# Kernel optimization log

Hardware: AMD Instinct MI355X
Metric: run time of the kernel (lower is better)

The kernel has to match this reference:

```python
import jax, jax.numpy as jnp
import numpy as np

DIM = 768


def setup_inputs() -> dict:
    key = jax.random.key(0)
    k1, k2, k3, k4, k5 = jax.random.split(key, 5)
    lines = jax.random.normal(k1, (32, 512, DIM), dtype=jnp.float32)
    videos = jax.random.normal(k2, (32, 128, DIM), dtype=jnp.float32)
    video_mask = jax.random.randint(k3, (32, 128), 0, 2, dtype=jnp.int32)
    # nn.Linear(dim, dim, bias=False) weights, applied as x @ W.T
    w_q = jax.random.normal(k4, (DIM, DIM), dtype=jnp.float32) * (DIM ** -0.5)
    w_k = jax.random.normal(k5, (DIM, DIM), dtype=jnp.float32) * (DIM ** -0.5)
    return {"lines": lines, "videos": videos, "video_mask": video_mask, "w_q": w_q, "w_k": w_k}


def reference(lines, videos, video_mask, w_q, w_k):
    scale = DIM ** -0.5
    q = jnp.einsum('bld,ed->ble', lines, w_q)   # (B, L, D)
    k = jnp.einsum('bvd,ed->bve', videos, w_k)  # (B, V, D)
    scores = jnp.einsum('bld,bvd->blv', q, k) * scale
    pad = (video_mask == 0)[:, None, :]          # (B, 1, V)
    scores = jnp.where(pad, jnp.float32(-1e9), scores)
    weights = jax.nn.softmax(scores, axis=-1)    # (B, L, V)
    return jnp.einsum('blv,bvd->bld', weights, videos)
```

## Files before the change

### kernel.cpp

```cpp
#include <hip/hip_runtime.h>

#define DIM 768
#define NB  32
#define LQ  512
#define NV  128

typedef unsigned short u16;
typedef unsigned int   u32;
typedef __bf16 bf16x8 __attribute__((ext_vector_type(8)));
typedef float  f32x4  __attribute__((ext_vector_type(4)));
typedef u16    u16x8  __attribute__((ext_vector_type(8)));
typedef u16    u16x4  __attribute__((ext_vector_type(4)));

typedef __attribute__((address_space(1))) const void gvoid;
typedef __attribute__((address_space(3))) void       svoid;

__device__ __forceinline__ u16 f2bf(float f) {
    u32 u = __float_as_uint(f);
    return (u16)((u + 0x7FFFu + ((u >> 16) & 1u)) >> 16);
}

__device__ __forceinline__ bf16x8 ld_frag(const u16* p) {
    return __builtin_bit_cast(bf16x8, *(const u16x8*)p);
}

__device__ __forceinline__ void gld16(const void* g, void* l) {
    __builtin_amdgcn_global_load_lds((gvoid*)g, (svoid*)l, 16, 0, 0);
}

#define NL_BLK 6144
#define NW_BLK 288

__device__ __forceinline__ void cvt_body(const float* __restrict__ src,
                                         u16* __restrict__ dst, int blk) {
    size_t i = (size_t)blk * 256 + threadIdx.x;
    float4 a = ((const float4*)src)[i * 2];
    float4 b = ((const float4*)src)[i * 2 + 1];
    u16x8 o = { f2bf(a.x), f2bf(a.y), f2bf(a.z), f2bf(a.w),
                f2bf(b.x), f2bf(b.y), f2bf(b.z), f2bf(b.w) };
    ((u16x8*)dst)[i] = o;
}

__global__ __launch_bounds__(256) void prep_kernel(const float* __restrict__ lines,
                                                   const float* __restrict__ w_q,
                                                   const float* __restrict__ w_k,
                                                   const float* __restrict__ videos,
                                                   u16* __restrict__ lbf,
                                                   u16* __restrict__ wqb,
                                                   u16* __restrict__ wkb,
                                                   u16* __restrict__ vt2,
                                                   u16* __restrict__ vbf) {
    __shared__ u16 T[64][136];
    const int bx = blockIdx.x;
    if (bx < NL_BLK)                 { cvt_body(lines, lbf, bx); return; }
    if (bx < NL_BLK + NW_BLK)        { cvt_body(w_q,   wqb, bx - NL_BLK); return; }
    if (bx < NL_BLK + 2 * NW_BLK)    { cvt_body(w_k,   wkb, bx - NL_BLK - NW_BLK); return; }

    const int v  = bx - (NL_BLK + 2 * NW_BLK);
    const int b  = v / 12;
    const int d0 = (v % 12) * 64;
    const int t  = threadIdx.x;
    const float* src = videos + (size_t)b * NV * DIM;
#pragma unroll
    for (int p = 0; p < 8; ++p) {
        int f  = t + p * 256;
        int vv = f >> 4;
        int c4 = f & 15;
        float4 x = *(const float4*)(src + (size_t)vv * DIM + d0 + c4 * 4);
        u16x4 o = { f2bf(x.x), f2bf(x.y), f2bf(x.z), f2bf(x.w) };
        T[c4 * 4 + 0][vv] = o[0];
        T[c4 * 4 + 1][vv] = o[1];
        T[c4 * 4 + 2][vv] = o[2];
        T[c4 * 4 + 3][vv] = o[3];
        *(u16x4*)(vbf + ((size_t)b * NV + vv) * DIM + d0 + c4 * 4) = o;
    }
    __syncthreads();
#pragma unroll
    for (int p = 0; p < 4; ++p) {
        int f  = t + p * 256;
        int dl = f >> 4;
        int v8 = f & 15;
        int d  = d0 + dl;
        int it = d >> 7, wv = (d >> 4) & 7, lnn = d & 15;
        int ks = v8 >> 2, qd = v8 & 3;
        int lane = qd * 16 + lnn;
        size_t off = ((((size_t)b * 6 + it) * 8 + wv) * 4 + ks) * 512 + lane * 8;
        *(u16x8*)(vt2 + off) = *(const u16x8*)&T[dl][v8 * 8];
    }
}

__global__ __launch_bounds__(512) void proj_kernel(const u16* __restrict__ A0,
                                                   const u16* __restrict__ W0,
                                                   u16* __restrict__ C0,
                                                   const u16* __restrict__ A1,
                                                   const u16* __restrict__ W1,
                                                   u16* __restrict__ C1) {
    __shared__ u16 sA[128][64];
    __shared__ u16 sB[128][64];
    const int t    = threadIdx.x;
    const int w    = t >> 6;
    const int lane = t & 63;
    const int quad = lane >> 4;
    const int ln   = lane & 15;

    const u16 *A, *W; u16 *C; int m0, n0;
    {
        int i = blockIdx.x;
        if (i < 768) { A = A0; W = W0; C = C0; }
        else         { A = A1; W = W1; C = C1; i -= 768; }
        int xcd = i & 7, s = i >> 3;
        m0 = ((s / 6) * 8 + xcd) * 128;
        n0 = (s % 6) * 128;
    }

    const int wr = (w >> 2) * 64;
    const int wc = (w & 3) * 32;
    const int srow   = lane >> 3;
    const int schunk = (lane & 7) ^ srow;

    f32x4 acc[4][2] = {};
#pragma unroll
    for (int ks = 0; ks < 12; ++ks) {
        __syncthreads();
#pragma unroll
        for (int p = 0; p < 2; ++p) {
            int rb = w * 16 + p * 8;
            gld16(A + (size_t)(m0 + rb + srow) * DIM + ks * 64 + schunk * 8, &sA[rb][0]);
            gld16(W + (size_t)(n0 + rb + srow) * DIM + ks * 64 + schunk * 8, &sB[rb][0]);
        }
        __syncthreads();
#pragma unroll
        for (int kk = 0; kk < 2; ++kk) {
            bf16x8 af[4], bfr[2];
#pragma unroll
            for (int i = 0; i < 4; ++i)
                af[i]  = ld_frag(&sA[wr + i * 16 + ln][((kk * 4 + quad) ^ (ln & 7)) * 8]);
#pragma unroll
            for (int j = 0; j < 2; ++j)
                bfr[j] = ld_frag(&sB[wc + j * 16 + ln][((kk * 4 + quad) ^ (ln & 7)) * 8]);
#pragma unroll
            for (int i = 0; i < 4; ++i)
#pragma unroll
                for (int j = 0; j < 2; ++j)
                    acc[i][j] = __builtin_amdgcn_mfma_f32_16x16x32_bf16(af[i], bfr[j], acc[i][j], 0, 0, 0);
        }
    }
#pragma unroll
    for (int i = 0; i < 4; ++i)
#pragma unroll
        for (int j = 0; j < 2; ++j)
#pragma unroll
            for (int r = 0; r < 4; ++r)
                C[(size_t)(m0 + wr + i * 16 + quad * 4 + r) * DIM + n0 + wc + j * 16 + ln] =
                    f2bf(acc[i][j][r]);
}

__global__ __launch_bounds__(512) void attn_kernel(const u16* __restrict__ Q,
                                                   const u16* __restrict__ K,
                                                   const u16* __restrict__ Vt2,
                                                   const int* __restrict__ mask,
                                                   float* __restrict__ out) {
    int b, l0;
    {
        int i = blockIdx.x;
        int xcd = i & 7, s = i >> 3;
        b  = (s >> 3) * 8 + xcd;
        l0 = (s & 7) * 64;
    }
    const int t    = threadIdx.x;
    const int w    = t >> 6;
    const int lane = t & 63;
    const int quad = lane >> 4;
    const int ln   = lane & 15;

    __shared__ union {
        struct { u16 q[64][64]; u16 k[128][64]; } st;
        float s[64][132];
    } uA;
    __shared__ union {
        struct { u16 q[64][64]; u16 k[128][64]; } st;
        u16 p[64][136];
    } uB;
    __shared__ float sBias[128];

    const u16* Qb = Q + ((size_t)b * LQ + l0) * DIM;
    const u16* Kb = K + (size_t)b * NV * DIM;
    if (t < NV) sBias[t] = mask[b * NV + t] ? 0.0f : -1e9f;

    const int srow   = lane >> 3;
    const int schunk = (lane & 7) ^ srow;

    auto stage = [&](int ks, int sel) {
        u16 (*q)[64] = sel ? uB.st.q : uA.st.q;
        u16 (*k)[64] = sel ? uB.st.k : uA.st.k;
        gld16(Qb + (size_t)(w * 8 + srow) * DIM + ks * 64 + schunk * 8, &q[w * 8][0]);
        gld16(Kb + (size_t)(w * 16 + srow) * DIM + ks * 64 + schunk * 8, &k[w * 16][0]);
        gld16(Kb + (size_t)(w * 16 + 8 + srow) * DIM + ks * 64 + schunk * 8, &k[w * 16 + 8][0]);
    };

    f32x4 accS[4] = {};
    stage(0, 0);
#pragma unroll
    for (int ks = 0; ks < 12; ++ks) {
        __syncthreads();
        if (ks < 11) stage(ks + 1, (ks + 1) & 1);
        u16 (*q)[64] = (ks & 1) ? uB.st.q : uA.st.q;
        u16 (*k)[64] = (ks & 1) ? uB.st.k : uA.st.k;
#pragma unroll
        for (int kk = 0; kk < 2; ++kk) {
            bf16x8 bfr = ld_frag(&k[w * 16 + ln][((kk * 4 + quad) ^ (ln & 7)) * 8]);
#pragma unroll
            for (int i = 0; i < 4; ++i) {
                bf16x8 af = ld_frag(&q[i * 16 + ln][((kk * 4 + quad) ^ (ln & 7)) * 8]);
                accS[i] = __builtin_amdgcn_mfma_f32_16x16x32_bf16(af, bfr, accS[i], 0, 0, 0);
            }
        }
    }
    __syncthreads();
    const float scale = 0.03608439182435161f;
#pragma unroll
    for (int i = 0; i < 4; ++i)
#pragma unroll
        for (int r = 0; r < 4; ++r)
            uA.s[i * 16 + quad * 4 + r][w * 16 + ln] = accS[i][r] * scale;
    __syncthreads();

    {
        const int row = t >> 3, seg = t & 7;
        float vals[16];
        float mx = -3.0e38f;
#pragma unroll
        for (int c = 0; c < 4; ++c) {
            float4 x  = *(const float4*)&uA.s[row][seg * 16 + c * 4];
            float4 bz = *(const float4*)&sBias[seg * 16 + c * 4];
            float a0 = x.x + bz.x, a1 = x.y + bz.y, a2 = x.z + bz.z, a3 = x.w + bz.w;
            vals[c * 4 + 0] = a0; vals[c * 4 + 1] = a1;
            vals[c * 4 + 2] = a2; vals[c * 4 + 3] = a3;
            mx = fmaxf(mx, fmaxf(fmaxf(a0, a1), fmaxf(a2, a3)));
        }
        mx = fmaxf(mx, __shfl_xor(mx, 1));
        mx = fmaxf(mx, __shfl_xor(mx, 2));
        mx = fmaxf(mx, __shfl_xor(mx, 4));
        float sum = 0.0f;
#pragma unroll
        for (int c = 0; c < 16; ++c) { float e = __expf(vals[c] - mx); vals[c] = e; sum += e; }
        sum += __shfl_xor(sum, 1);
        sum += __shfl_xor(sum, 2);
        sum += __shfl_xor(sum, 4);
        const float inv = 1.0f / sum;
        __syncthreads();
#pragma unroll
        for (int h = 0; h < 2; ++h) {
            u16x8 pk;
#pragma unroll
            for (int e = 0; e < 8; ++e) pk[e] = f2bf(vals[h * 8 + e] * inv);
            *(u16x8*)&uB.p[row][seg * 16 + h * 8] = pk;
        }
    }
    __syncthreads();

    bf16x8 paf[4][4];
#pragma unroll
    for (int i = 0; i < 4; ++i)
#pragma unroll
        for (int ks = 0; ks < 4; ++ks)
            paf[i][ks] = ld_frag(&uB.p[i * 16 + ln][ks * 32 + quad * 8]);

    const u16* V2 = Vt2 + (size_t)b * 6 * 8 * 4 * 512;
    float*     Ob = out + ((size_t)b * LQ + l0) * DIM;
    for (int it = 0; it < 6; ++it) {
        f32x4 accO[4] = {};
#pragma unroll
        for (int ks = 0; ks < 4; ++ks) {
            bf16x8 bv = ld_frag(V2 + (((size_t)(it * 8 + w)) * 4 + ks) * 512 + lane * 8);
#pragma unroll
            for (int i = 0; i < 4; ++i)
                accO[i] = __builtin_amdgcn_mfma_f32_16x16x32_bf16(paf[i][ks], bv, accO[i], 0, 0, 0);
        }
#pragma unroll
        for (int i = 0; i < 4; ++i)
#pragma unroll
            for (int r = 0; r < 4; ++r)
                Ob[(size_t)(i * 16 + quad * 4 + r) * DIM + it * 128 + w * 16 + ln] = accO[i][r];
    }
}

extern "C" void kernel_launch(void* const* d_in, const int* in_sizes, int n_in,
                              void* d_out, int out_size, void* d_ws, size_t ws_size,
                              hipStream_t stream) {
    const float* lines  = (const float*)d_in[0];
    const float* videos = (const float*)d_in[1];
    const int*   mask   = (const int*)d_in[2];
    const float* w_q    = (const float*)d_in[3];
    const float* w_k    = (const float*)d_in[4];
    float*       out    = (float*)d_out;

    u16* qw  = (u16*)d_ws;
    u16* kw  = qw  + (size_t)NB * LQ * DIM;
    u16* vt2 = kw  + (size_t)NB * NV * DIM;
    u16* lbf = vt2 + (size_t)NB * DIM * NV;
    u16* vbf = lbf + (size_t)NB * LQ * DIM;
    u16* wqb = vbf + (size_t)NB * NV * DIM;
    u16* wkb = wqb + (size_t)DIM * DIM;

    prep_kernel<<<NL_BLK + 2 * NW_BLK + 384, 256, 0, stream>>>(
        lines, w_q, w_k, videos, lbf, wqb, wkb, vt2, vbf);
    proj_kernel<<<960, 512, 0, stream>>>(lbf, wqb, qw, vbf, wkb, kw);
    attn_kernel<<<256, 512, 0, stream>>>(qw, kw, vt2, mask, out);
}
```

Before: 168.5 us.

## Fold Wq^T Wk into one matrix and project only videos

Scores are reassociated as lines · (Wq^T Wk · videos^T). A 768x768 combined weight is computed in the prep kernel from transposed fp32 tiles, then a smaller GEMM projects only the videos (B*128 rows) with that weight, and attention uses the raw bf16 lines as queries. This removes the large lines projection GEMM (B*512 rows). In exchange, the weight product is rounded to bf16, which adds a second rounding step that changes precision, and the few blocks computing the weight product may become a long tail in prep.

```diff
diff --git a/kernel.cpp b/kernel.cpp
--- a/kernel.cpp
+++ b/kernel.cpp
@@ -28,38 +28,92 @@
     __builtin_amdgcn_global_load_lds((gvoid*)g, (svoid*)l, 16, 0, 0);
 }
 
+#define W2_BLK 36
 #define NL_BLK 6144
-#define NW_BLK 288
-
-__device__ __forceinline__ void cvt_body(const float* __restrict__ src,
-                                         u16* __restrict__ dst, int blk) {
-    size_t i = (size_t)blk * 256 + threadIdx.x;
-    float4 a = ((const float4*)src)[i * 2];
-    float4 b = ((const float4*)src)[i * 2 + 1];
-    u16x8 o = { f2bf(a.x), f2bf(a.y), f2bf(a.z), f2bf(a.w),
-                f2bf(b.x), f2bf(b.y), f2bf(b.z), f2bf(b.w) };
-    ((u16x8*)dst)[i] = o;
-}
 
 __global__ __launch_bounds__(256) void prep_kernel(const float* __restrict__ lines,
                                                    const float* __restrict__ w_q,
                                                    const float* __restrict__ w_k,
                                                    const float* __restrict__ videos,
                                                    u16* __restrict__ lbf,
-                                                   u16* __restrict__ wqb,
-                                                   u16* __restrict__ wkb,
+                                                   u16* __restrict__ w2b,
                                                    u16* __restrict__ vt2,
                                                    u16* __restrict__ vbf) {
-    __shared__ u16 T[64][136];
+    __shared__ union {
+        u16 T[64][136];
+        struct { u16 q[128][72]; u16 k[128][72]; } w2s;
+    } uL;
     const int bx = blockIdx.x;
-    if (bx < NL_BLK)                 { cvt_body(lines, lbf, bx); return; }
-    if (bx < NL_BLK + NW_BLK)        { cvt_body(w_q,   wqb, bx - NL_BLK); return; }
-    if (bx < NL_BLK + 2 * NW_BLK)    { cvt_body(w_k,   wkb, bx - NL_BLK - NW_BLK); return; }
-
-    const int v  = bx - (NL_BLK + 2 * NW_BLK);
+    const int t  = threadIdx.x;
+
+    if (bx < W2_BLK) {
+        const int m0 = (bx / 6) * 128;
+        const int n0 = (bx % 6) * 128;
+        const int w    = t >> 6;
+        const int lane = t & 63;
+        const int quad = lane >> 4;
+        const int ln   = lane & 15;
+        const int wr   = (w >> 1) * 64;
+        const int wc   = (w & 1) * 64;
+        f32x4 acc[4][4] = {};
+        for (int ks = 0; ks < 12; ++ks) {
+            __syncthreads();
+            const int e0 = ks * 64;
+#pragma unroll
+            for (int p = 0; p < 8; ++p) {
+                int f  = t + p * 256;
+                int r  = f >> 5;
+                int c4 = f & 31;
+                float4 xq = *(const float4*)(w_q + (size_t)(e0 + r) * DIM + m0 + c4 * 4);
+                float4 xk = *(const float4*)(w_k + (size_t)(e0 + r) * DIM + n0 + c4 * 4);
+                uL.w2s.q[c4 * 4 + 0][r] = f2bf(xq.x);
+                uL.w2s.q[c4 * 4 + 1][r] = f2bf(xq.y);
+                uL.w2s.q[c4 * 4 + 2][r] = f2bf(xq.z);
+                uL.w2s.q[c4 * 4 + 3][r] = f2bf(xq.w);
+                uL.w2s.k[c4 * 4 + 0][r] = f2bf(xk.x);
+                uL.w2s.k[c4 * 4 + 1][r] = f2bf(xk.y);
+                uL.w2s.k[c4 * 4 + 2][r] = f2bf(xk.z);
+                uL.w2s.k[c4 * 4 + 3][r] = f2bf(xk.w);
+            }
+            __syncthreads();
+#pragma unroll
+            for (int kk = 0; kk < 2; ++kk) {
+                bf16x8 af[4], bfr[4];
+#pragma unroll
+                for (int i = 0; i < 4; ++i) af[i]  = ld_frag(&uL.w2s.q[wr + i * 16 + ln][kk * 32 + quad * 8]);
+#pragma unroll
+                for (int j = 0; j < 4; ++j) bfr[j] = ld_frag(&uL.w2s.k[wc + j * 16 + ln][kk * 32 + quad * 8]);
+#pragma unroll
+                for (int i = 0; i < 4; ++i)
+#pragma unroll
+                    for (int j = 0; j < 4; ++j)
+                        acc[i][j] = __builtin_amdgcn_mfma_f32_16x16x32_bf16(af[i], bfr[j], acc[i][j], 0, 0, 0);
+            }
+        }
+#pragma unroll
+        for (int i = 0; i < 4; ++i)
+#pragma unroll
+            for (int j = 0; j < 4; ++j)
+#pragma unroll
+                for (int r = 0; r < 4; ++r)
+                    w2b[(size_t)(m0 + wr + i * 16 + quad * 4 + r) * DIM + n0 + wc + j * 16 + ln] =
+                        f2bf(acc[i][j][r]);
+        return;
+    }
+
+    if (bx < W2_BLK + NL_BLK) {
+        size_t i = (size_t)(bx - W2_BLK) * 256 + t;
+        float4 a = ((const float4*)lines)[i * 2];
+        float4 b = ((const float4*)lines)[i * 2 + 1];
+        u16x8 o = { f2bf(a.x), f2bf(a.y), f2bf(a.z), f2bf(a.w),
+                    f2bf(b.x), f2bf(b.y), f2bf(b.z), f2bf(b.w) };
+        ((u16x8*)lbf)[i] = o;
+        return;
+    }
+
+    const int v  = bx - (W2_BLK + NL_BLK);
     const int b  = v / 12;
     const int d0 = (v % 12) * 64;
-    const int t  = threadIdx.x;
     const float* src = videos + (size_t)b * NV * DIM;
 #pragma unroll
     for (int p = 0; p < 8; ++p) {
@@ -68,10 +122,10 @@
         int c4 = f & 15;
         float4 x = *(const float4*)(src + (size_t)vv * DIM + d0 + c4 * 4);
         u16x4 o = { f2bf(x.x), f2bf(x.y), f2bf(x.z), f2bf(x.w) };
-        T[c4 * 4 + 0][vv] = o[0];
-        T[c4 * 4 + 1][vv] = o[1];
-        T[c4 * 4 + 2][vv] = o[2];
-        T[c4 * 4 + 3][vv] = o[3];
+        uL.T[c4 * 4 + 0][vv] = o[0];
+        uL.T[c4 * 4 + 1][vv] = o[1];
+        uL.T[c4 * 4 + 2][vv] = o[2];
+        uL.T[c4 * 4 + 3][vv] = o[3];
         *(u16x4*)(vbf + ((size_t)b * NV + vv) * DIM + d0 + c4 * 4) = o;
     }
     __syncthreads();
@@ -85,16 +139,13 @@
         int ks = v8 >> 2, qd = v8 & 3;
         int lane = qd * 16 + lnn;
         size_t off = ((((size_t)b * 6 + it) * 8 + wv) * 4 + ks) * 512 + lane * 8;
-        *(u16x8*)(vt2 + off) = *(const u16x8*)&T[dl][v8 * 8];
-    }
-}
-
-__global__ __launch_bounds__(512) void proj_kernel(const u16* __restrict__ A0,
-                                                   const u16* __restrict__ W0,
-                                                   u16* __restrict__ C0,
-                                                   const u16* __restrict__ A1,
-                                                   const u16* __restrict__ W1,
-                                                   u16* __restrict__ C1) {
+        *(u16x8*)(vt2 + off) = *(const u16x8*)&uL.T[dl][v8 * 8];
+    }
+}
+
+__global__ __launch_bounds__(512) void g_kernel(const u16* __restrict__ A,
+                                                const u16* __restrict__ W,
+                                                u16* __restrict__ C) {
     __shared__ u16 sA[128][64];
     __shared__ u16 sB[128][64];
     const int t    = threadIdx.x;
@@ -103,11 +154,9 @@
     const int quad = lane >> 4;
     const int ln   = lane & 15;
 
-    const u16 *A, *W; u16 *C; int m0, n0;
+    int m0, n0;
     {
         int i = blockIdx.x;
-        if (i < 768) { A = A0; W = W0; C = C0; }
-        else         { A = A1; W = W1; C = C1; i -= 768; }
         int xcd = i & 7, s = i >> 3;
         m0 = ((s / 6) * 8 + xcd) * 128;
         n0 = (s % 6) * 128;
@@ -295,16 +344,14 @@
     const float* w_k    = (const float*)d_in[4];
     float*       out    = (float*)d_out;
 
-    u16* qw  = (u16*)d_ws;
-    u16* kw  = qw  + (size_t)NB * LQ * DIM;
-    u16* vt2 = kw  + (size_t)NB * NV * DIM;
+    u16* gw  = (u16*)d_ws;
+    u16* vt2 = gw  + (size_t)NB * NV * DIM;
     u16* lbf = vt2 + (size_t)NB * DIM * NV;
     u16* vbf = lbf + (size_t)NB * LQ * DIM;
-    u16* wqb = vbf + (size_t)NB * NV * DIM;
-    u16* wkb = wqb + (size_t)DIM * DIM;
-
-    prep_kernel<<<NL_BLK + 2 * NW_BLK + 384, 256, 0, stream>>>(
-        lines, w_q, w_k, videos, lbf, wqb, wkb, vt2, vbf);
-    proj_kernel<<<960, 512, 0, stream>>>(lbf, wqb, qw, vbf, wkb, kw);
-    attn_kernel<<<256, 512, 0, stream>>>(qw, kw, vt2, mask, out);
-}
+    u16* w2b = vbf + (size_t)NB * NV * DIM;
+
+    prep_kernel<<<W2_BLK + NL_BLK + 384, 256, 0, stream>>>(
+        lines, w_q, w_k, videos, lbf, w2b, vt2, vbf);
+    g_kernel   <<<192, 512, 0, stream>>>(vbf, w2b, gw);
+    attn_kernel<<<256, 512, 0, stream>>>(lbf, gw, vt2, mask, out);
+}
```

Result: slower. 192.6 us (+14.3%).
